# Kernel optimization log

Measured on AMD Instinct MI355X. Metric: run time of the kernel, lower is better.

The kernel has to match this reference:

```python
import jax, jax.numpy as jnp
import numpy as np

B, S, D, H, F = 4, 1024, 1024, 16, 4096
DH = D // H
EPS = 1e-5


def _ln(x, g, b):
    mu = jnp.mean(x, axis=-1, keepdims=True)
    var = jnp.mean((x - mu) ** 2, axis=-1, keepdims=True)
    return (x - mu) * jax.lax.rsqrt(var + EPS) * g + b


def _mha(q_in, k_in, v_in, mask, wq, bq, wk, bk, wv, bv, wo, bo):
    b, sq, d = q_in.shape
    sk = k_in.shape[1]
    Q = (q_in @ wq + bq).reshape(b, sq, H, DH).transpose(0, 2, 1, 3)  # [B,H,Sq,dh]
    K = (k_in @ wk + bk).reshape(b, sk, H, DH).transpose(0, 2, 1, 3)
    V = (v_in @ wv + bv).reshape(b, sk, H, DH).transpose(0, 2, 1, 3)
    scores = jnp.einsum('bhqd,bhkd->bhqk', Q, K) / jnp.sqrt(jnp.asarray(DH, Q.dtype))
    if mask is not None:
        scores = jnp.where(mask[:, None] == 0, jnp.asarray(-1e9, scores.dtype), scores)
    w = jax.nn.softmax(scores, axis=-1)
    ctx = jnp.einsum('bhqk,bhkd->bhqd', w, V).transpose(0, 2, 1, 3).reshape(b, sq, d)
    return ctx @ wo + bo


def setup_inputs() -> dict:
    key = jax.random.key(0)
    ks = jax.random.split(key, 20)
    s = 0.02
    inp = {
        'x': jax.random.normal(ks[0], (B, S, D), jnp.float32),
        'src_x': jax.random.normal(ks[1], (B, S, D), jnp.float32),
        # causal self-attention mask (1 = keep), cross mask all ones
        'mask': jnp.broadcast_to(jnp.tril(jnp.ones((S, S), jnp.int32)), (B, S, S)),
        'src_mask': jnp.ones((B, S, S), jnp.int32),
        'ln1_g': jnp.ones((D,), jnp.float32), 'ln1_b': jnp.zeros((D,), jnp.float32),
        'ln2_g': jnp.ones((D,), jnp.float32), 'ln2_b': jnp.zeros((D,), jnp.float32),
        'ln3_g': jnp.ones((D,), jnp.float32), 'ln3_b': jnp.zeros((D,), jnp.float32),
    }
    names = ['sa_wq', 'sa_wk', 'sa_wv', 'sa_wo', 'ca_wq', 'ca_wk', 'ca_wv', 'ca_wo']
    for i, n in enumerate(names):
        inp[n] = jax.random.normal(ks[2 + i], (D, D), jnp.float32) * s
        inp[n.replace('w', 'b')] = jnp.zeros((D,), jnp.float32)
    inp['ff_w1'] = jax.random.normal(ks[10], (D, F), jnp.float32) * s
    inp['ff_b1'] = jnp.zeros((F,), jnp.float32)
    inp['ff_w2'] = jax.random.normal(ks[11], (F, D), jnp.float32) * s
    inp['ff_b2'] = jnp.zeros((D,), jnp.float32)
    return inp


def reference(x, mask, src_x, src_mask,
              ln1_g, ln1_b, ln2_g, ln2_b, ln3_g, ln3_b,
              sa_wq, sa_bq, sa_wk, sa_bk, sa_wv, sa_bv, sa_wo, sa_bo,
              ca_wq, ca_bq, ca_wk, ca_bk, ca_wv, ca_bv, ca_wo, ca_bo,
              ff_w1, ff_b1, ff_w2, ff_b2):
    # pre-layer-norm decoder layer (dropout = 0 / eval mode)
    h = _ln(x, ln1_g, ln1_b)
    x = x + _mha(h, h, h, mask, sa_wq, sa_bq, sa_wk, sa_bk, sa_wv, sa_bv, sa_wo, sa_bo)
    h = _ln(x, ln2_g, ln2_b)
    x = x + _mha(h, src_x, src_x, src_mask, ca_wq, ca_bq, ca_wk, ca_bk, ca_wv, ca_bv, ca_wo, ca_bo)
    h = _ln(x, ln3_g, ln3_b)
    x = x + (jax.nn.relu(h @ ff_w1 + ff_b1) @ ff_w2 + ff_b2)
    return x
```

## Files before the change

kernel.cpp:

```cpp
#include <hip/hip_runtime.h>
#include <hip/hip_bf16.h>

#define B_ 4
#define S_ 1024
#define D_ 1024
#define H_ 16
#define DH_ 64
#define F_ 4096

typedef unsigned short u16;
typedef unsigned int u32;
typedef __attribute__((ext_vector_type(8))) short bf16x8;
typedef __attribute__((ext_vector_type(4))) short bf16x4;
typedef __attribute__((ext_vector_type(4))) float f32x4;

__device__ __forceinline__ float bf2f(u16 u) {
    return __uint_as_float(((u32)u) << 16);
}
__device__ __forceinline__ u16 f2bf(float f) {
    __hip_bfloat16 h = __float2bfloat16(f);
    return *reinterpret_cast<u16*>(&h);
}

typedef __attribute__((address_space(1))) const u32 gu32;
typedef __attribute__((address_space(3))) u32 lu32;
__device__ __forceinline__ void gl_lds16(const void* g, void* l) {
    __builtin_amdgcn_global_load_lds((gu32*)g, (lu32*)l, 16, 0, 0);
}

__global__ __launch_bounds__(256) void cvt1_kernel(const float* __restrict__ s,
                                                   u16* __restrict__ d) {
    int i = (blockIdx.x * 256 + threadIdx.x) * 4;
    float4 v = *(const float4*)(s + i);
    u16 o0 = f2bf(v.x), o1 = f2bf(v.y), o2 = f2bf(v.z), o3 = f2bf(v.w);
    d[i] = o0; d[i+1] = o1; d[i+2] = o2; d[i+3] = o3;
}

__device__ __forceinline__ void trcvt_body(const float* __restrict__ src,
                                           u16* __restrict__ dst, int K, int N,
                                           int n0, int k0) {
    __shared__ u16 tile[64][65];
    int t = threadIdx.x;
    int c = t & 63, r4 = t >> 6;
#pragma unroll
    for (int i = 0; i < 16; i++) {
        int r = i * 4 + r4;
        tile[c][r] = f2bf(src[(size_t)(k0 + r) * N + n0 + c]);
    }
    __syncthreads();
#pragma unroll
    for (int i = 0; i < 16; i++) {
        int rr = i * 4 + r4;
        dst[(size_t)(n0 + rr) * K + k0 + c] = tile[rr][c];
    }
}

__global__ __launch_bounds__(256) void trcvt_kernel(const float* __restrict__ src,
                                                    u16* __restrict__ dst,
                                                    int K, int N) {
    trcvt_body(src, dst, K, N, blockIdx.x * 64, blockIdx.y * 64);
}

struct TP { const float* src[8]; u16* dst[8]; };
__global__ __launch_bounds__(256) void trcvt8_kernel(TP tp) {
    trcvt_body(tp.src[blockIdx.z], tp.dst[blockIdx.z], D_, D_,
               blockIdx.x * 64, blockIdx.y * 64);
}

__global__ __launch_bounds__(256) void mask_reduce_kernel(const int* __restrict__ mask,
                                                          unsigned char* __restrict__ bmask) {
    int t = threadIdx.x;
    int qb = blockIdx.x >> 4, kb = blockIdx.x & 15, b = blockIdx.y;
    bool all1 = true, any1 = false;
#pragma unroll
    for (int i = 0; i < 16; i++) {
        int e = t + i * 256;
        int r = e >> 6, c = e & 63;
        int v = mask[((size_t)(b * S_ + qb * 64 + r)) * S_ + kb * 64 + c];
        all1 = all1 && (v != 0);
        any1 = any1 || (v != 0);
    }
    unsigned long long ba = __ballot(all1), bn = __ballot(any1);
    __shared__ unsigned long long sa[4], sn[4];
    if ((t & 63) == 0) { sa[t >> 6] = ba; sn[t >> 6] = bn; }
    __syncthreads();
    if (t == 0) {
        bool A = ((sa[0] & sa[1] & sa[2] & sa[3]) == ~0ull);
        bool Y = ((sn[0] | sn[1] | sn[2] | sn[3]) != 0ull);
        bmask[b * 256 + blockIdx.x] = A ? 2 : (Y ? 1 : 0);
    }
}

template<bool COPY>
__global__ __launch_bounds__(256) void ln_kernel(const float* __restrict__ xin,
                                                 const float* __restrict__ g,
                                                 const float* __restrict__ bta,
                                                 float* xcur,
                                                 u16* __restrict__ hout) {
    int row = blockIdx.x;
    int t = threadIdx.x;
    size_t base = (size_t)row * D_;
    float v[4];
#pragma unroll
    for (int i = 0; i < 4; i++) v[i] = xin[base + t + i * 256];
    float s  = v[0] + v[1] + v[2] + v[3];
    float s2 = v[0]*v[0] + v[1]*v[1] + v[2]*v[2] + v[3]*v[3];
#pragma unroll
    for (int m = 1; m < 64; m <<= 1) {
        s  += __shfl_xor(s, m);
        s2 += __shfl_xor(s2, m);
    }
    __shared__ float red[8];
    int wave = t >> 6;
    if ((t & 63) == 0) { red[wave*2] = s; red[wave*2+1] = s2; }
    __syncthreads();
    float fs  = red[0] + red[2] + red[4] + red[6];
    float fs2 = red[1] + red[3] + red[5] + red[7];
    float mu  = fs * (1.0f / D_);
    float var = fs2 * (1.0f / D_) - mu * mu;
    float rs  = rsqrtf(var + 1e-5f);
#pragma unroll
    for (int i = 0; i < 4; i++) {
        int c = t + i * 256;
        float x = v[i];
        if (COPY) xcur[base + c] = x;
        hout[base + c] = f2bf((x - mu) * rs * g[c] + bta[c]);
    }
}

struct Bias3 { const float* b0; const float* b1; const float* b2; int n1; int n2; };

__device__ __forceinline__ float bias_at(const Bias3& bs, int c) {
    const float* p; int o;
    if (c < bs.n1)      { p = bs.b0; o = c; }
    else if (c < bs.n2) { p = bs.b1; o = c - bs.n1; }
    else                { p = bs.b2; o = c - bs.n2; }
    return p[o];
}

template<int BM, int BN, int OUT_MODE, bool BIAS_ROW>
__device__ __forceinline__ void gemm128_body(const u16* __restrict__ A,
                                             const u16* __restrict__ Bt,
                                             Bias3 bias,
                                             const float* res,
                                             void* out,
                                             int M, int N, int K,
                                             int lda, int ldb) {
    constexpr int MT = (BM == 64) ? 4 : (BN == 64 ? 2 : 4);
    constexpr int NT = (BN == 64) ? 4 : (BM == 64 ? 2 : 4);
    __shared__ u16 As[2][BM * 64];
    __shared__ u16 Bs[2][BN * 64];
    int t = threadIdx.x;
    int m0 = blockIdx.y * BM, n0 = blockIdx.x * BN;
    int w = t >> 6, lane = t & 63, quad = lane >> 4, l16 = lane & 15;
    int wm, wn;
    if (BM == 128 && BN == 128) { wm = (w >> 1) * 64; wn = (w & 1) * 64; }
    else if (BN == 64)          { wm = w * 32;        wn = 0; }
    else                        { wm = 0;             wn = w * 32; }

    f32x4 acc[MT][NT] = {};
    int sr = lane >> 3;
    int gc = ((lane & 7) ^ sr) * 8;
    int x7 = l16 & 7;
    const u16* gA = A + (size_t)m0 * lda;
    const u16* gB = Bt + (size_t)n0 * ldb;

    auto stage = [&](int k0, int buf) {
#pragma unroll
        for (int j = w; j < BM / 8; j += 4)
            gl_lds16(gA + (size_t)(j * 8 + sr) * lda + k0 + gc, &As[buf][j * 512]);
#pragma unroll
        for (int j = w; j < BN / 8; j += 4)
            gl_lds16(gB + (size_t)(j * 8 + sr) * ldb + k0 + gc, &Bs[buf][j * 512]);
    };

    stage(0, 0);
    int cur = 0;
    for (int k0 = 0; k0 < K; k0 += 64) {
        __syncthreads();
        if (k0 + 64 < K) stage(k0 + 64, cur ^ 1);

#pragma unroll
        for (int s = 0; s < 2; s++) {
            bf16x8 af[MT], bfr[NT];
            int cp = ((s * 4 + quad) ^ x7) * 8;
#pragma unroll
            for (int mt = 0; mt < MT; mt++)
                af[mt] = *(const bf16x8*)&As[cur][(wm + mt * 16 + l16) * 64 + cp];
#pragma unroll
            for (int nt = 0; nt < NT; nt++)
                bfr[nt] = *(const bf16x8*)&Bs[cur][(wn + nt * 16 + l16) * 64 + cp];
#pragma unroll
            for (int mt = 0; mt < MT; mt++)
#pragma unroll
                for (int nt = 0; nt < NT; nt++)
                    acc[mt][nt] = __builtin_amdgcn_mfma_f32_16x16x32_bf16(af[mt], bfr[nt], acc[mt][nt], 0, 0, 0);
        }
        cur ^= 1;
    }

#pragma unroll
    for (int nt = 0; nt < NT; nt++) {
        int col = n0 + wn + nt * 16 + l16;
        float bc = (OUT_MODE == 3) ? 0.f : (BIAS_ROW ? 0.f : bias_at(bias, col));
#pragma unroll
        for (int mt = 0; mt < MT; mt++) {
#pragma unroll
            for (int r = 0; r < 4; r++) {
                int row = m0 + wm + mt * 16 + quad * 4 + r;
                float v = acc[mt][nt][r] + bc;
                if (OUT_MODE != 3 && BIAS_ROW) v += bias_at(bias, row);
                if (OUT_MODE == 1) v = fmaxf(v, 0.f);
                if (OUT_MODE == 2) {
                    v += res[(size_t)row * N + col];
                    ((float*)out)[(size_t)row * N + col] = v;
                } else if (OUT_MODE == 3) {
                    ((float*)out)[(size_t)row * N + col] = v;
                } else {
                    ((u16*)out)[(size_t)row * N + col] = f2bf(v);
                }
            }
        }
    }
}

template<int BM, int BN, int OUT_MODE, bool BIAS_ROW>
__global__ __launch_bounds__(256) void gemm128_kernel(const u16* __restrict__ A,
                                                      const u16* __restrict__ Bt,
                                                      Bias3 bias,
                                                      const float* res,
                                                      void* out,
                                                      int M, int N, int K) {
    gemm128_body<BM, BN, OUT_MODE, BIAS_ROW>(A, Bt, bias, res, out, M, N, K, K, K);
}

__global__ __launch_bounds__(256) void gemm128_splitk2_kernel(const u16* __restrict__ A,
                                                              const u16* __restrict__ Bt,
                                                              float* __restrict__ p0,
                                                              float* __restrict__ p1,
                                                              int M, int N, int Kh, int ld) {
    int z = blockIdx.z;
    Bias3 dummy = { nullptr, nullptr, nullptr, 1 << 30, 1 << 30 };
    gemm128_body<128, 128, 3, false>(A + z * Kh, Bt + z * Kh, dummy, nullptr,
                                     z ? (void*)p1 : (void*)p0, M, N, Kh, ld, ld);
}

__global__ __launch_bounds__(256) void ffn2_reduce_kernel(const float* __restrict__ p0,
                                                          const float* __restrict__ p1,
                                                          const float* __restrict__ b2,
                                                          const float* __restrict__ res,
                                                          float* __restrict__ out) {
    int i = (blockIdx.x * 256 + threadIdx.x) * 4;
    int col = i & (D_ - 1);
    float4 a = *(const float4*)(p0 + i);
    float4 b = *(const float4*)(p1 + i);
    float4 r = *(const float4*)(res + i);
    float4 bb = *(const float4*)(b2 + col);
    float4 o;
    o.x = a.x + b.x + r.x + bb.x;
    o.y = a.y + b.y + r.y + bb.y;
    o.z = a.z + b.z + r.z + bb.z;
    o.w = a.w + b.w + r.w + bb.w;
    *(float4*)(out + i) = o;
}

struct Pair2 {
    const u16* A0; const u16* A1;
    const u16* B0; const u16* B1;
    const float* b0; const float* b1;
    u16* o0; u16* o1;
};
__global__ __launch_bounds__(256) void gemm128_pairqk_kernel(Pair2 p, int M, int N, int K) {
    int z = blockIdx.z;
    const u16* A  = z ? p.A1 : p.A0;
    const u16* Bt = z ? p.B1 : p.B0;
    const float* bb = z ? p.b1 : p.b0;
    u16* o = z ? p.o1 : p.o0;
    Bias3 bs = { bb, bb, bb, 1 << 30, 1 << 30 };
    gemm128_body<128, 64, 0, false>(A, Bt, bs, nullptr, o, M, N, K, K, K);
}

__global__ __launch_bounds__(256) void attn_kernel(const u16* __restrict__ Q, int ldq,
                                                   const u16* __restrict__ Kb, int ldk,
                                                   const u16* __restrict__ Vt,
                                                   const int* __restrict__ mask,
                                                   const unsigned char* __restrict__ bmask,
                                                   u16* __restrict__ ctx) {
    __shared__ u16 Ks[2][2][64 * 64];
    __shared__ u16 Vs[2][2][64 * 64];
    int t = threadIdx.x;
    int b = blockIdx.z, hh = blockIdx.y;
    int w = t >> 6, lane = t & 63, quad = lane >> 4, l16 = lane & 15;
    int hoff = hh * DH_;

    int qt[2] = { (int)blockIdx.x, 15 - (int)blockIdx.x };

    bf16x8 ones8;
#pragma unroll
    for (int j = 0; j < 8; j++) ones8[j] = (short)0x3F80;

    bf16x8 qf[2][2];
#pragma unroll
    for (int tt = 0; tt < 2; tt++) {
        int qrow = qt[tt] * 64 + w * 16 + l16;
#pragma unroll
        for (int kk = 0; kk < 2; kk++) {
            bf16x8 v = *(const bf16x8*)(Q + (size_t)(b * S_ + qrow) * ldq + hoff + kk * 32 + quad * 8);
#pragma unroll
            for (int j = 0; j < 8; j++)
                v[j] = (short)f2bf(bf2f((u16)v[j]) * 0.125f);
            qf[tt][kk] = v;
        }
    }

    f32x4 oacc[2][4] = {};
    f32x4 lacc[2] = {};

    unsigned nz[2], mx[2];
#pragma unroll
    for (int tt = 0; tt < 2; tt++) {
        nz[tt] = 0; mx[tt] = 0;
        for (int c = 0; c < 16; c++) {
            int v = bmask ? (int)bmask[(b * 16 + qt[tt]) * 16 + c] : 1;
            if (v)      nz[tt] |= 1u << c;
            if (v == 1) mx[tt] |= 1u << c;
        }
    }
    unsigned nzU = nz[0] | nz[1];
    unsigned remS = 0;
    for (int s = 0; s < 8; s++) if ((nzU >> (2 * s)) & 3u) remS |= 1u << s;

    int sr = lane >> 3;
    int gc = ((lane & 7) ^ sr) * 8;

    auto stage64 = [&](int c, int buf) {
        int k0 = c * 64, c64 = c & 1;
        for (int j = w; j < 8; j += 4) {
            gl_lds16(Kb + (size_t)(b * S_ + k0 + j * 8 + sr) * ldk + hoff + gc, &Ks[buf][c64][j * 512]);
            gl_lds16(Vt + (size_t)(hoff + j * 8 + sr) * (B_ * S_) + b * S_ + k0 + gc, &Vs[buf][c64][j * 512]);
        }
    };
    auto stageS = [&](int s, int buf) {
        if ((nzU >> (2 * s)) & 1u)     stage64(2 * s, buf);
        if ((nzU >> (2 * s + 1)) & 1u) stage64(2 * s + 1, buf);
    };

    int cur = 0;
    int s = remS ? __builtin_ctz(remS) : 8;
    if (s < 8) stageS(s, 0);

    while (s < 8) {
        remS &= remS - 1;
        int ns = remS ? __builtin_ctz(remS) : 8;
        __syncthreads();
        if (ns < 8) stageS(ns, cur ^ 1);

#pragma unroll
        for (int c64 = 0; c64 < 2; c64++) {
            int c = 2 * s + c64;
            if (!((nzU >> c) & 1u)) continue;
            int k0c = c * 64;
            const u16* KsT = &Ks[cur][c64][0];
            const u16* VsT = &Vs[cur][c64][0];

#pragma unroll
            for (int tt = 0; tt < 2; tt++) {
                if (!((nz[tt] >> c) & 1u)) continue;
                bool mixed = (mx[tt] >> c) & 1u;

                float p[4][4];
#pragma unroll
                for (int nt = 0; nt < 4; nt++) {
                    f32x4 sacc = {};
                    int krow = nt * 16 + l16;
                    __builtin_amdgcn_s_setprio(1);
#pragma unroll
                    for (int kk = 0; kk < 2; kk++) {
                        int cp = ((kk * 4 + quad) ^ (krow & 7)) * 8;
                        bf16x8 kf = *(const bf16x8*)&KsT[krow * 64 + cp];
                        sacc = __builtin_amdgcn_mfma_f32_16x16x32_bf16(kf, qf[tt][kk], sacc, 0, 0, 0);
                    }
                    __builtin_amdgcn_s_setprio(0);
#pragma unroll
                    for (int r = 0; r < 4; r++) {
                        float sv = sacc[r];
                        if (mixed) {
                            int qq = qt[tt] * 64 + w * 16 + l16;
                            int kc = k0c + nt * 16 + quad * 4 + r;
                            if (mask[(size_t)(b * S_ + qq) * S_ + kc] == 0) sv = -1e9f;
                        }
                        p[nt][r] = __expf(fminf(sv, 20.f));
                    }
                }

#pragma unroll
                for (int mp = 0; mp < 2; mp++) {
                    bf16x8 af;
#pragma unroll
                    for (int r = 0; r < 4; r++) {
                        af[r]     = (short)f2bf(p[2 * mp][r]);
                        af[4 + r] = (short)f2bf(p[2 * mp + 1][r]);
                    }
                    __builtin_amdgcn_s_setprio(1);
                    lacc[tt] = __builtin_amdgcn_mfma_f32_16x16x32_bf16(af, ones8, lacc[tt], 0, 0, 0);
#pragma unroll
                    for (int dt = 0; dt < 4; dt++) {
                        int vrow = dt * 16 + l16;
                        int ch0 = ((2 * mp) * 2 + (quad >> 1)) ^ (vrow & 7);
                        int ch1 = ((2 * mp + 1) * 2 + (quad >> 1)) ^ (vrow & 7);
                        int off = (quad & 1) * 4;
                        bf16x4 lo = *(const bf16x4*)&VsT[vrow * 64 + ch0 * 8 + off];
                        bf16x4 hi = *(const bf16x4*)&VsT[vrow * 64 + ch1 * 8 + off];
                        bf16x8 vf;
#pragma unroll
                        for (int j = 0; j < 4; j++) { vf[j] = lo[j]; vf[4 + j] = hi[j]; }
                        oacc[tt][dt] = __builtin_amdgcn_mfma_f32_16x16x32_bf16(af, vf, oacc[tt][dt], 0, 0, 0);
                    }
                    __builtin_amdgcn_s_setprio(0);
                }
            }
        }
        s = ns;
        cur ^= 1;
    }

#pragma unroll
    for (int tt = 0; tt < 2; tt++)
#pragma unroll
        for (int dt = 0; dt < 4; dt++)
#pragma unroll
            for (int r = 0; r < 4; r++) {
                int qq = qt[tt] * 64 + w * 16 + quad * 4 + r;
                float l = lacc[tt][r];
                float inv = l > 0.f ? 1.f / l : 0.f;
                ctx[(size_t)(b * S_ + qq) * D_ + hoff + dt * 16 + l16] = f2bf(oacc[tt][dt][r] * inv);
            }
}

extern "C" void kernel_launch(void* const* d_in, const int* in_sizes, int n_in,
                              void* d_out, int out_size, void* d_ws, size_t ws_size,
                              hipStream_t stream) {
    const float* x     = (const float*)d_in[0];
    const float* srcx  = (const float*)d_in[1];
    const int*   mask  = (const int*)d_in[2];
    const int*   smask = (const int*)d_in[3];
    const float* ln1g = (const float*)d_in[4],  *ln1b = (const float*)d_in[5];
    const float* ln2g = (const float*)d_in[6],  *ln2b = (const float*)d_in[7];
    const float* ln3g = (const float*)d_in[8],  *ln3b = (const float*)d_in[9];
    const float* sa_wq = (const float*)d_in[10], *sa_bq = (const float*)d_in[11];
    const float* sa_wk = (const float*)d_in[12], *sa_bk = (const float*)d_in[13];
    const float* sa_wv = (const float*)d_in[14], *sa_bv = (const float*)d_in[15];
    const float* sa_wo = (const float*)d_in[16], *sa_bo = (const float*)d_in[17];
    const float* ca_wq = (const float*)d_in[18], *ca_bq = (const float*)d_in[19];
    const float* ca_wk = (const float*)d_in[20], *ca_bk = (const float*)d_in[21];
    const float* ca_wv = (const float*)d_in[22], *ca_bv = (const float*)d_in[23];
    const float* ca_wo = (const float*)d_in[24], *ca_bo = (const float*)d_in[25];
    const float* ff_w1 = (const float*)d_in[26], *ff_b1 = (const float*)d_in[27];
    const float* ff_w2 = (const float*)d_in[28], *ff_b2 = (const float*)d_in[29];

    char* ws = (char*)d_ws;
    const size_t MB = 1ull << 20;
    const size_t DD = (size_t)D_ * D_;
    float* xcur = (float*)ws;
    u16* h     = (u16*)(ws + 16 * MB);
    u16* qk    = (u16*)(ws + 24 * MB);
    u16* qb    = (u16*)(ws + 24 * MB);
    u16* kbuf  = (u16*)(ws + 32 * MB);
    u16* vt    = (u16*)(ws + 40 * MB);
    u16* ctx   = (u16*)(ws + 48 * MB);
    u16* ff    = (u16*)(ws + 24 * MB);
    u16* sxb   = (u16*)(ws + 56 * MB);
    u16* wqk_s = (u16*)(ws + 64 * MB);
    u16* wv_s  = (u16*)(ws + 68 * MB);
    u16* wo_s  = (u16*)(ws + 70 * MB);
    u16* wq_c  = (u16*)(ws + 72 * MB);
    u16* wk_c  = (u16*)(ws + 74 * MB);
    u16* wv_c  = (u16*)(ws + 76 * MB);
    u16* wo_c  = (u16*)(ws + 78 * MB);
    u16* wff1  = (u16*)(ws + 80 * MB);
    u16* wff2  = (u16*)(ws + 88 * MB);
    float* fp0 = (float*)(ws + 56 * MB);
    float* fp1 = (float*)(ws + 72 * MB);
    unsigned char* bm_self = nullptr, *bm_cross = nullptr;
    if (ws_size >= 96 * MB + 8192) {
        bm_self  = (unsigned char*)(ws + ws_size - 8192);
        bm_cross = bm_self + 4096;
    }

    dim3 blk(256);

    TP tp = {{sa_wq, sa_wk, sa_wv, sa_wo, ca_wq, ca_wk, ca_wv, ca_wo},
             {wqk_s, wqk_s + DD, wv_s, wo_s, wq_c, wk_c, wv_c, wo_c}};
    trcvt8_kernel<<<dim3(16, 16, 8), blk, 0, stream>>>(tp);
    trcvt_kernel<<<dim3(F_ / 64, D_ / 64), blk, 0, stream>>>(ff_w1, wff1, D_, F_);
    trcvt_kernel<<<dim3(D_ / 64, F_ / 64), blk, 0, stream>>>(ff_w2, wff2, F_, D_);
    cvt1_kernel<<<B_ * S_ * D_ / 1024, blk, 0, stream>>>(srcx, sxb);
    if (bm_self) {
        mask_reduce_kernel<<<dim3(256, B_), blk, 0, stream>>>(mask, bm_self);
        mask_reduce_kernel<<<dim3(256, B_), blk, 0, stream>>>(smask, bm_cross);
    }

    Bias3 bqk = { sa_bq, sa_bk, sa_bk, 1024, 2048 };
    Bias3 bsv = { sa_bv, sa_bv, sa_bv, 1 << 30, 1 << 30 };
    Bias3 bso = { sa_bo, sa_bo, sa_bo, 1 << 30, 1 << 30 };
    Bias3 bcv = { ca_bv, ca_bv, ca_bv, 1 << 30, 1 << 30 };
    Bias3 bco = { ca_bo, ca_bo, ca_bo, 1 << 30, 1 << 30 };
    Bias3 bf1 = { ff_b1, ff_b1, ff_b1, 1 << 30, 1 << 30 };

    ln_kernel<true><<<B_ * S_, blk, 0, stream>>>(x, ln1g, ln1b, xcur, h);
    gemm128_kernel<128,128,0,false><<<dim3(16, 32), blk, 0, stream>>>(h, wqk_s, bqk, nullptr, qk, 4096, 2048, 1024);
    gemm128_kernel<64,128,0,true><<<dim3(32, 16), blk, 0, stream>>>(wv_s, h, bsv, nullptr, vt, 1024, 4096, 1024);
    attn_kernel<<<dim3(8, H_, B_), blk, 0, stream>>>(qk, 2048, qk + 1024, 2048, vt, mask, bm_self, ctx);
    gemm128_kernel<128,64,2,false><<<dim3(16, 32), blk, 0, stream>>>(ctx, wo_s, bso, xcur, xcur, 4096, 1024, 1024);

    ln_kernel<false><<<B_ * S_, blk, 0, stream>>>(xcur, ln2g, ln2b, nullptr, h);
    {
        Pair2 pqk = { h, sxb, wq_c, wk_c, ca_bq, ca_bk, qb, kbuf };
        gemm128_pairqk_kernel<<<dim3(16, 32, 2), blk, 0, stream>>>(pqk, 4096, 1024, 1024);
    }
    gemm128_kernel<64,128,0,true><<<dim3(32, 16), blk, 0, stream>>>(wv_c, sxb, bcv, nullptr, vt, 1024, 4096, 1024);
    attn_kernel<<<dim3(8, H_, B_), blk, 0, stream>>>(qb, 1024, kbuf, 1024, vt, smask, bm_cross, ctx);
    gemm128_kernel<128,64,2,false><<<dim3(16, 32), blk, 0, stream>>>(ctx, wo_c, bco, xcur, xcur, 4096, 1024, 1024);

    ln_kernel<false><<<B_ * S_, blk, 0, stream>>>(xcur, ln3g, ln3b, nullptr, h);
    gemm128_kernel<128,128,1,false><<<dim3(32, 32), blk, 0, stream>>>(h, wff1, bf1, nullptr, ff, 4096, 4096, 1024);
    gemm128_splitk2_kernel<<<dim3(8, 32, 2), blk, 0, stream>>>(ff, wff2, fp0, fp1, 4096, 1024, 2048, 4096);
    ffn2_reduce_kernel<<<dim3(B_ * S_ * D_ / 1024), blk, 0, stream>>>(fp0, fp1, ff_b2, xcur, (float*)d_out);
}
```

Baseline: 566.8 us.

## Permute V^T columns in GEMM epilogue and use one query tile per attention block

The V-projection GEMM gains an output mode that writes V^T with its key columns permuted inside each 64-wide group. The attention kernel can then load each V fragment with a single 16-byte LDS read instead of two 8-byte reads. The attention kernel also drops the paired causal query tiles (qt and 15-qt per block) and launches one 64-row query tile per block, doubling the grid and halving LDS use. The trade-off is losing the balanced causal work per block and the shared K/V staging across two tiles, in return for more blocks and simpler, cheaper inner loops.

```diff
diff --git a/kernel.cpp b/kernel.cpp
--- a/kernel.cpp
+++ b/kernel.cpp
@@ -216,6 +216,10 @@
                     ((float*)out)[(size_t)row * N + col] = v;
                 } else if (OUT_MODE == 3) {
                     ((float*)out)[(size_t)row * N + col] = v;
+                } else if (OUT_MODE == 4) {
+                    int pc = (col & ~63) | (col & 32) | ((col & 0xC) << 1) |
+                             ((col & 0x10) >> 2) | (col & 3);
+                    ((u16*)out)[(size_t)row * N + pc] = f2bf(v);
                 } else {
                     ((u16*)out)[(size_t)row * N + col] = f2bf(v);
                 }
@@ -286,155 +290,121 @@
                                                    const int* __restrict__ mask,
                                                    const unsigned char* __restrict__ bmask,
                                                    u16* __restrict__ ctx) {
-    __shared__ u16 Ks[2][2][64 * 64];
-    __shared__ u16 Vs[2][2][64 * 64];
+    __shared__ u16 Ks[2][64 * 64];
+    __shared__ u16 Vs[2][64 * 64];
     int t = threadIdx.x;
-    int b = blockIdx.z, hh = blockIdx.y;
+    int b = blockIdx.z, hh = blockIdx.y, qt = blockIdx.x;
     int w = t >> 6, lane = t & 63, quad = lane >> 4, l16 = lane & 15;
     int hoff = hh * DH_;
 
-    int qt[2] = { (int)blockIdx.x, 15 - (int)blockIdx.x };
-
     bf16x8 ones8;
 #pragma unroll
     for (int j = 0; j < 8; j++) ones8[j] = (short)0x3F80;
 
-    bf16x8 qf[2][2];
-#pragma unroll
-    for (int tt = 0; tt < 2; tt++) {
-        int qrow = qt[tt] * 64 + w * 16 + l16;
-#pragma unroll
-        for (int kk = 0; kk < 2; kk++) {
-            bf16x8 v = *(const bf16x8*)(Q + (size_t)(b * S_ + qrow) * ldq + hoff + kk * 32 + quad * 8);
-#pragma unroll
-            for (int j = 0; j < 8; j++)
-                v[j] = (short)f2bf(bf2f((u16)v[j]) * 0.125f);
-            qf[tt][kk] = v;
-        }
-    }
-
-    f32x4 oacc[2][4] = {};
-    f32x4 lacc[2] = {};
-
-    unsigned nz[2], mx[2];
-#pragma unroll
-    for (int tt = 0; tt < 2; tt++) {
-        nz[tt] = 0; mx[tt] = 0;
-        for (int c = 0; c < 16; c++) {
-            int v = bmask ? (int)bmask[(b * 16 + qt[tt]) * 16 + c] : 1;
-            if (v)      nz[tt] |= 1u << c;
-            if (v == 1) mx[tt] |= 1u << c;
-        }
-    }
-    unsigned nzU = nz[0] | nz[1];
-    unsigned remS = 0;
-    for (int s = 0; s < 8; s++) if ((nzU >> (2 * s)) & 3u) remS |= 1u << s;
+    bf16x8 qf[2];
+    int qrow = qt * 64 + w * 16 + l16;
+#pragma unroll
+    for (int kk = 0; kk < 2; kk++) {
+        bf16x8 v = *(const bf16x8*)(Q + (size_t)(b * S_ + qrow) * ldq + hoff + kk * 32 + quad * 8);
+#pragma unroll
+        for (int j = 0; j < 8; j++)
+            v[j] = (short)f2bf(bf2f((u16)v[j]) * 0.125f);
+        qf[kk] = v;
+    }
+
+    f32x4 oacc[4] = {};
+    f32x4 lacc = {};
+
+    unsigned nz = 0, mx = 0;
+    for (int c = 0; c < 16; c++) {
+        int v = bmask ? (int)bmask[(b * 16 + qt) * 16 + c] : 1;
+        if (v)      nz |= 1u << c;
+        if (v == 1) mx |= 1u << c;
+    }
 
     int sr = lane >> 3;
     int gc = ((lane & 7) ^ sr) * 8;
 
     auto stage64 = [&](int c, int buf) {
-        int k0 = c * 64, c64 = c & 1;
+        int k0 = c * 64;
         for (int j = w; j < 8; j += 4) {
-            gl_lds16(Kb + (size_t)(b * S_ + k0 + j * 8 + sr) * ldk + hoff + gc, &Ks[buf][c64][j * 512]);
-            gl_lds16(Vt + (size_t)(hoff + j * 8 + sr) * (B_ * S_) + b * S_ + k0 + gc, &Vs[buf][c64][j * 512]);
+            gl_lds16(Kb + (size_t)(b * S_ + k0 + j * 8 + sr) * ldk + hoff + gc, &Ks[buf][j * 512]);
+            gl_lds16(Vt + (size_t)(hoff + j * 8 + sr) * (B_ * S_) + b * S_ + k0 + gc, &Vs[buf][j * 512]);
         }
     };
-    auto stageS = [&](int s, int buf) {
-        if ((nzU >> (2 * s)) & 1u)     stage64(2 * s, buf);
-        if ((nzU >> (2 * s + 1)) & 1u) stage64(2 * s + 1, buf);
-    };
-
+
+    unsigned rem = nz;
+    int c = rem ? __builtin_ctz(rem) : -1;
+    if (c >= 0) stage64(c, 0);
     int cur = 0;
-    int s = remS ? __builtin_ctz(remS) : 8;
-    if (s < 8) stageS(s, 0);
-
-    while (s < 8) {
-        remS &= remS - 1;
-        int ns = remS ? __builtin_ctz(remS) : 8;
+
+    while (c >= 0) {
+        rem &= rem - 1;
+        int nc = rem ? __builtin_ctz(rem) : -1;
         __syncthreads();
-        if (ns < 8) stageS(ns, cur ^ 1);
-
-#pragma unroll
-        for (int c64 = 0; c64 < 2; c64++) {
-            int c = 2 * s + c64;
-            if (!((nzU >> c) & 1u)) continue;
-            int k0c = c * 64;
-            const u16* KsT = &Ks[cur][c64][0];
-            const u16* VsT = &Vs[cur][c64][0];
-
-#pragma unroll
-            for (int tt = 0; tt < 2; tt++) {
-                if (!((nz[tt] >> c) & 1u)) continue;
-                bool mixed = (mx[tt] >> c) & 1u;
-
-                float p[4][4];
-#pragma unroll
-                for (int nt = 0; nt < 4; nt++) {
-                    f32x4 sacc = {};
-                    int krow = nt * 16 + l16;
-                    __builtin_amdgcn_s_setprio(1);
-#pragma unroll
-                    for (int kk = 0; kk < 2; kk++) {
-                        int cp = ((kk * 4 + quad) ^ (krow & 7)) * 8;
-                        bf16x8 kf = *(const bf16x8*)&KsT[krow * 64 + cp];
-                        sacc = __builtin_amdgcn_mfma_f32_16x16x32_bf16(kf, qf[tt][kk], sacc, 0, 0, 0);
-                    }
-                    __builtin_amdgcn_s_setprio(0);
-#pragma unroll
-                    for (int r = 0; r < 4; r++) {
-                        float sv = sacc[r];
-                        if (mixed) {
-                            int qq = qt[tt] * 64 + w * 16 + l16;
-                            int kc = k0c + nt * 16 + quad * 4 + r;
-                            if (mask[(size_t)(b * S_ + qq) * S_ + kc] == 0) sv = -1e9f;
-                        }
-                        p[nt][r] = __expf(fminf(sv, 20.f));
-                    }
+        if (nc >= 0) stage64(nc, cur ^ 1);
+
+        int k0c = c * 64;
+        bool mixed = (mx >> c) & 1u;
+        const u16* KsT = Ks[cur];
+        const u16* VsT = Vs[cur];
+
+        float p[4][4];
+#pragma unroll
+        for (int nt = 0; nt < 4; nt++) {
+            f32x4 sacc = {};
+            int krow = nt * 16 + l16;
+            __builtin_amdgcn_s_setprio(1);
+#pragma unroll
+            for (int kk = 0; kk < 2; kk++) {
+                int cp = ((kk * 4 + quad) ^ (krow & 7)) * 8;
+                bf16x8 kf = *(const bf16x8*)&KsT[krow * 64 + cp];
+                sacc = __builtin_amdgcn_mfma_f32_16x16x32_bf16(kf, qf[kk], sacc, 0, 0, 0);
+            }
+            __builtin_amdgcn_s_setprio(0);
+#pragma unroll
+            for (int r = 0; r < 4; r++) {
+                float sv = sacc[r];
+                if (mixed) {
+                    int kc = k0c + nt * 16 + quad * 4 + r;
+                    if (mask[(size_t)(b * S_ + qrow) * S_ + kc] == 0) sv = -1e9f;
                 }
-
-#pragma unroll
-                for (int mp = 0; mp < 2; mp++) {
-                    bf16x8 af;
-#pragma unroll
-                    for (int r = 0; r < 4; r++) {
-                        af[r]     = (short)f2bf(p[2 * mp][r]);
-                        af[4 + r] = (short)f2bf(p[2 * mp + 1][r]);
-                    }
-                    __builtin_amdgcn_s_setprio(1);
-                    lacc[tt] = __builtin_amdgcn_mfma_f32_16x16x32_bf16(af, ones8, lacc[tt], 0, 0, 0);
-#pragma unroll
-                    for (int dt = 0; dt < 4; dt++) {
-                        int vrow = dt * 16 + l16;
-                        int ch0 = ((2 * mp) * 2 + (quad >> 1)) ^ (vrow & 7);
-                        int ch1 = ((2 * mp + 1) * 2 + (quad >> 1)) ^ (vrow & 7);
-                        int off = (quad & 1) * 4;
-                        bf16x4 lo = *(const bf16x4*)&VsT[vrow * 64 + ch0 * 8 + off];
-                        bf16x4 hi = *(const bf16x4*)&VsT[vrow * 64 + ch1 * 8 + off];
-                        bf16x8 vf;
-#pragma unroll
-                        for (int j = 0; j < 4; j++) { vf[j] = lo[j]; vf[4 + j] = hi[j]; }
-                        oacc[tt][dt] = __builtin_amdgcn_mfma_f32_16x16x32_bf16(af, vf, oacc[tt][dt], 0, 0, 0);
-                    }
-                    __builtin_amdgcn_s_setprio(0);
-                }
+                p[nt][r] = __expf(fminf(sv, 20.f));
             }
         }
-        s = ns;
+
+#pragma unroll
+        for (int mp = 0; mp < 2; mp++) {
+            bf16x8 af;
+#pragma unroll
+            for (int r = 0; r < 4; r++) {
+                af[r]     = (short)f2bf(p[2 * mp][r]);
+                af[4 + r] = (short)f2bf(p[2 * mp + 1][r]);
+            }
+            __builtin_amdgcn_s_setprio(1);
+            lacc = __builtin_amdgcn_mfma_f32_16x16x32_bf16(af, ones8, lacc, 0, 0, 0);
+#pragma unroll
+            for (int dt = 0; dt < 4; dt++) {
+                int vrow = dt * 16 + l16;
+                int ch = (mp * 4 + quad) ^ (vrow & 7);
+                bf16x8 vf = *(const bf16x8*)&VsT[vrow * 64 + ch * 8];
+                oacc[dt] = __builtin_amdgcn_mfma_f32_16x16x32_bf16(af, vf, oacc[dt], 0, 0, 0);
+            }
+            __builtin_amdgcn_s_setprio(0);
+        }
+        c = nc;
         cur ^= 1;
     }
 
 #pragma unroll
-    for (int tt = 0; tt < 2; tt++)
-#pragma unroll
-        for (int dt = 0; dt < 4; dt++)
-#pragma unroll
-            for (int r = 0; r < 4; r++) {
-                int qq = qt[tt] * 64 + w * 16 + quad * 4 + r;
-                float l = lacc[tt][r];
-                float inv = l > 0.f ? 1.f / l : 0.f;
-                ctx[(size_t)(b * S_ + qq) * D_ + hoff + dt * 16 + l16] = f2bf(oacc[tt][dt][r] * inv);
-            }
+    for (int dt = 0; dt < 4; dt++)
+#pragma unroll
+        for (int r = 0; r < 4; r++) {
+            int qq = qt * 64 + w * 16 + quad * 4 + r;
+            float l = lacc[r];
+            float inv = l > 0.f ? 1.f / l : 0.f;
+            ctx[(size_t)(b * S_ + qq) * D_ + hoff + dt * 16 + l16] = f2bf(oacc[dt][r] * inv);
+        }
 }
 
 extern "C" void kernel_launch(void* const* d_in, const int* in_sizes, int n_in,
@@ -509,8 +479,8 @@
 
     ln_kernel<true><<<B_ * S_, blk, 0, stream>>>(x, ln1g, ln1b, xcur, h);
     gemm128_kernel<128,128,0,false><<<dim3(16, 32), blk, 0, stream>>>(h, wqk_s, bqk, nullptr, qk, 4096, 2048, 1024);
-    gemm128_kernel<64,128,0,true><<<dim3(32, 16), blk, 0, stream>>>(wv_s, h, bsv, nullptr, vt, 1024, 4096, 1024);
-    attn_kernel<<<dim3(8, H_, B_), blk, 0, stream>>>(qk, 2048, qk + 1024, 2048, vt, mask, bm_self, ctx);
+    gemm128_kernel<64,128,4,true><<<dim3(32, 16), blk, 0, stream>>>(wv_s, h, bsv, nullptr, vt, 1024, 4096, 1024);
+    attn_kernel<<<dim3(16, H_, B_), blk, 0, stream>>>(qk, 2048, qk + 1024, 2048, vt, mask, bm_self, ctx);
     gemm128_kernel<128,64,2,false><<<dim3(16, 32), blk, 0, stream>>>(ctx, wo_s, bso, xcur, xcur, 4096, 1024, 1024);
 
     ln_kernel<false><<<B_ * S_, blk, 0, stream>>>(xcur, ln2g, ln2b, nullptr, h);
@@ -518,8 +488,8 @@
         Pair2 pqk = { h, sxb, wq_c, wk_c, ca_bq, ca_bk, qb, kbuf };
         gemm128_pairqk_kernel<<<dim3(16, 32, 2), blk, 0, stream>>>(pqk, 4096, 1024, 1024);
     }
-    gemm128_kernel<64,128,0,true><<<dim3(32, 16), blk, 0, stream>>>(wv_c, sxb, bcv, nullptr, vt, 1024, 4096, 1024);
-    attn_kernel<<<dim3(8, H_, B_), blk, 0, stream>>>(qb, 1024, kbuf, 1024, vt, smask, bm_cross, ctx);
+    gemm128_kernel<64,128,4,true><<<dim3(32, 16), blk, 0, stream>>>(wv_c, sxb, bcv, nullptr, vt, 1024, 4096, 1024);
+    attn_kernel<<<dim3(16, H_, B_), blk, 0, stream>>>(qb, 1024, kbuf, 1024, vt, smask, bm_cross, ctx);
     gemm128_kernel<128,64,2,false><<<dim3(16, 32), blk, 0, stream>>>(ctx, wo_c, bco, xcur, xcur, 4096, 1024, 1024);
 
     ln_kernel<false><<<B_ * S_, blk, 0, stream>>>(xcur, ln3g, ln3b, nullptr, h);
```

Result: faster. 553.2 us (-2.4%).
